# Optimization experiments

Hardware: AMD Instinct MI355X
Metric: run time of the kernel (lower is better)

The kernel has to match this reference:

```python
import jax, jax.numpy as jnp
import numpy as np

TOP_K = 2
EPS = 1e-9


def setup_inputs() -> dict:
    key = jax.random.key(0)
    ks = jax.random.split(key, 5)
    B, S, D, H, E, G = 4, 2048, 1024, 1024, 8, 256
    x = jax.random.normal(ks[0], (B, S, D), dtype=jnp.float32)
    # gate MLP (top_k_gating with hidden_size=gating_size)
    Wg1 = jax.random.normal(ks[1], (D, G), dtype=jnp.float32) * (1.0 / np.sqrt(D))
    Wg2 = jax.random.normal(ks[2], (G, E), dtype=jnp.float32) * (1.0 / np.sqrt(G))
    # experts: uniform(-1/D, 1/D) as in init_experts
    W_in = jax.random.uniform(ks[3], (E, D, H), dtype=jnp.float32, minval=-1.0 / D, maxval=1.0 / D)
    W_out = jax.random.uniform(ks[4], (E, H, D), dtype=jnp.float32, minval=-1.0 / D, maxval=1.0 / D)
    return {"x": x, "Wg1": Wg1, "Wg2": Wg2, "W_in": W_in, "W_out": W_out}


def _gate(xf, Wg1, Wg2):
    # gate MLP -> softmax probs over experts
    h = jnp.tanh(xf @ Wg1)                      # [N, G]
    probs = jax.nn.softmax(h @ Wg2, axis=-1)    # [N, E]
    top_v, top_i = jax.lax.top_k(probs, TOP_K)  # [N, k]
    N, E = probs.shape
    # dense gate matrix: zeros except top-k entries (== compute_gating combine weights)
    gates = jnp.zeros((N, E), probs.dtype).at[jnp.arange(N)[:, None], top_i].set(top_v)
    return gates, probs


def _mi_loss(probs):
    # mutual-information aux loss: minimize -(H(mean_p) - mean H(p))
    p_mean = probs.mean(axis=0)
    h_mean = -jnp.sum(p_mean * jnp.log(p_mean + EPS))
    mean_h = -jnp.mean(jnp.sum(probs * jnp.log(probs + EPS), axis=-1))
    return -h_mean + mean_h


def reference(x, Wg1, Wg2, W_in, W_out):
    B, S, D = x.shape
    xf = x.reshape(-1, D)                        # [N, D]
    gates, probs = _gate(xf, Wg1, Wg2)           # [N, E]
    # per-expert FFN: relu(x @ W_in[e]) @ W_out[e], combined with top-k gates.
    h = jnp.einsum('nd,edh->enh', xf, W_in)      # [E, N, H]
    h = jax.nn.relu(h)
    y = jnp.einsum('enh,ehd->end', h, W_out)     # [E, N, D]
    out = jnp.einsum('ne,end->nd', gates, y)     # gate-weighted combine
    loss = _mi_loss(probs)
    return out.reshape(B, S, D), loss
```

## Files before the change

kernel.cpp:

```cpp
#include <hip/hip_runtime.h>


#define N_TOK 8192
#define DIM   1024
#define HID   1024
#define NEXP  8
#define GDIM  256
#define NPAIR (N_TOK * 2)
#define HB_ROWS (NPAIR + 256)
#define MT2   72
#define GAP_P 5e-4f
#define SPLIT_SCALE 2048.0f

typedef __attribute__((ext_vector_type(4))) float    f32x4;
typedef __attribute__((ext_vector_type(8))) _Float16 f16x8;

static __device__ __forceinline__ void async_ld16(const void* g, void* l) {
  __builtin_amdgcn_global_load_lds(
      (const __attribute__((address_space(1))) unsigned int*)g,
      (__attribute__((address_space(3))) unsigned int*)l, 16, 0, 0);
}

__global__ void cast_x_kernel(const float* __restrict__ x, _Float16* __restrict__ xh,
                              _Float16* __restrict__ xl) {
  size_t o = ((size_t)blockIdx.x * 256 + threadIdx.x) * 8;
  float4 v0 = *(const float4*)(x + o);
  float4 v1 = *(const float4*)(x + o + 4);
  float v[8] = {v0.x, v0.y, v0.z, v0.w, v1.x, v1.y, v1.z, v1.w};
  f16x8 h, l;
#pragma unroll
  for (int k = 0; k < 8; ++k) {
    _Float16 hi = (_Float16)v[k];
    h[k] = hi;
    l[k] = (_Float16)((v[k] - (float)hi) * SPLIT_SCALE);
  }
  *(f16x8*)(xh + o) = h;
  *(f16x8*)(xl + o) = l;
}

__global__ __launch_bounds__(256) void cast_wg1_kernel(const float* __restrict__ Wg1,
                                                       _Float16* __restrict__ WhT,
                                                       _Float16* __restrict__ WlT) {
  __shared__ float t[64][65];
  int k0 = blockIdx.x * 64, g0 = blockIdx.y * 64;
  int tid = threadIdx.x;
  int col4 = tid & 15, ib = tid >> 4;
#pragma unroll
  for (int q = 0; q < 4; ++q) {
    int i = ib * 4 + q;
    *(float4*)&t[i][col4 * 4] = *(const float4*)&Wg1[(size_t)(k0 + i) * GDIM + g0 + col4 * 4];
  }
  __syncthreads();
#pragma unroll
  for (int q = 0; q < 2; ++q) {
    int c = tid * 2 + q;
    int j = c >> 3, i8 = (c & 7) * 8;
    f16x8 h, l;
#pragma unroll
    for (int k = 0; k < 8; ++k) {
      float v = t[i8 + k][j];
      _Float16 hi = (_Float16)v;
      h[k] = hi;
      l[k] = (_Float16)((v - (float)hi) * SPLIT_SCALE);
    }
    *(f16x8*)&WhT[(size_t)(g0 + j) * DIM + k0 + i8] = h;
    *(f16x8*)&WlT[(size_t)(g0 + j) * DIM + k0 + i8] = l;
  }
}

__global__ __launch_bounds__(256) void cast_wT_kernel(const float* __restrict__ Win,
                                                      const float* __restrict__ Wout,
                                                      _Float16* __restrict__ WinT,
                                                      _Float16* __restrict__ WoutT) {
  __shared__ float t[64][65];
  int z = blockIdx.z;
  const float* src = (z < NEXP ? Win : Wout) + (size_t)(z & 7) * DIM * HID;
  _Float16*    dst = (z < NEXP ? WinT : WoutT) + (size_t)(z & 7) * DIM * HID;
  int i0 = blockIdx.x * 64, j0 = blockIdx.y * 64;
  int tid = threadIdx.x;
  int col4 = tid & 15, ib = tid >> 4;
#pragma unroll
  for (int q = 0; q < 4; ++q) {
    int i = ib * 4 + q;
    *(float4*)&t[i][col4 * 4] = *(const float4*)&src[(size_t)(i0 + i) * 1024 + j0 + col4 * 4];
  }
  __syncthreads();
#pragma unroll
  for (int q = 0; q < 2; ++q) {
    int c = tid * 2 + q;
    int j = c >> 3, i8 = (c & 7) * 8;
    f16x8 h;
#pragma unroll
    for (int k = 0; k < 8; ++k) h[k] = (_Float16)t[i8 + k][j];
    *(f16x8*)&dst[(size_t)(j0 + j) * 1024 + i0 + i8] = h;
  }
}

__global__ __launch_bounds__(256) void gemm_hm_kernel(const _Float16* __restrict__ xh,
                                                      const _Float16* __restrict__ xl,
                                                      const _Float16* __restrict__ WhT,
                                                      const _Float16* __restrict__ WlT,
                                                      float* __restrict__ hg) {
  __shared__ __align__(16) _Float16 Ah[32 * 32], Al[32 * 32];
  __shared__ __align__(16) _Float16 Bh[128 * 32], Bl[128 * 32];
  int m0 = blockIdx.x * 32, n0 = blockIdx.y * 128;
  int tid = threadIdx.x, lane = tid & 63, wave = tid >> 6;
  int wr = (wave >> 1) * 16, wc = (wave & 1) * 64;
  int sel = tid >> 7, tt = tid & 127;
  int arow = tt >> 2;
  int aslot = (tt & 3) ^ ((tt >> 4) & 3);
  const _Float16* asrcp = (sel ? xl : xh) + (size_t)(m0 + arow) * DIM + aslot * 8;
  _Float16* adst = (sel ? Al : Ah) + (size_t)tt * 8;
  int brow = tid >> 2;
  int bslot = (tid & 3) ^ ((tid >> 4) & 3);
  size_t boff = (size_t)(n0 + brow) * DIM + bslot * 8;
  const size_t bo2 = (size_t)64 * DIM;
  int rdoff = ((lane >> 4) ^ ((lane >> 2) & 3)) << 3;
  f32x4 acc[4] = {}, accl[4] = {};
  for (int k0 = 0; k0 < DIM; k0 += 32) {
    __syncthreads();
    async_ld16(asrcp + k0, adst);
    async_ld16(WhT + boff + k0, Bh + (size_t)tid * 8);
    async_ld16(WhT + boff + bo2 + k0, Bh + (size_t)(256 + tid) * 8);
    async_ld16(WlT + boff + k0, Bl + (size_t)tid * 8);
    async_ld16(WlT + boff + bo2 + k0, Bl + (size_t)(256 + tid) * 8);
    __syncthreads();
    f16x8 a  = *(const f16x8*)&Ah[(wr + (lane & 15)) * 32 + rdoff];
    f16x8 al = *(const f16x8*)&Al[(wr + (lane & 15)) * 32 + rdoff];
#pragma unroll
    for (int n = 0; n < 4; ++n) {
      f16x8 b  = *(const f16x8*)&Bh[(wc + n * 16 + (lane & 15)) * 32 + rdoff];
      f16x8 bl = *(const f16x8*)&Bl[(wc + n * 16 + (lane & 15)) * 32 + rdoff];
      acc[n]  = __builtin_amdgcn_mfma_f32_16x16x32_f16(a, b, acc[n], 0, 0, 0);
      accl[n] = __builtin_amdgcn_mfma_f32_16x16x32_f16(al, b, accl[n], 0, 0, 0);
      accl[n] = __builtin_amdgcn_mfma_f32_16x16x32_f16(a, bl, accl[n], 0, 0, 0);
    }
  }
#pragma unroll
  for (int n = 0; n < 4; ++n) {
#pragma unroll
    for (int i = 0; i < 4; ++i) {
      int row = wr + ((lane >> 4) << 2) + i;
      int col = wc + n * 16 + (lane & 15);
      float v = acc[n][i] + accl[n][i] * (1.0f / SPLIT_SCALE);
      hg[(size_t)(m0 + row) * GDIM + n0 + col] = tanhf(v);
    }
  }
}

__global__ void gate_kernel(const float* __restrict__ hg, const float* __restrict__ Wg2,
                            int* __restrict__ top_i, float* __restrict__ top_v,
                            float* __restrict__ lossacc, int* __restrict__ counts,
                            int* __restrict__ nflag, int* __restrict__ flaglist) {
  __shared__ float psum[8];
  __shared__ float entsum;
  __shared__ int cnts[8];
  int tid = threadIdx.x;
  if (tid < 8) { psum[tid] = 0.f; cnts[tid] = 0; }
  if (tid == 0) entsum = 0.f;
  __syncthreads();
  int token = blockIdx.x * 8 + (tid >> 5);
  int lane = tid & 31;
  const float* hrow = hg + (size_t)token * GDIM;
  float lg[8] = {0, 0, 0, 0, 0, 0, 0, 0};
#pragma unroll
  for (int j = 0; j < 8; ++j) {
    int g = lane + (j << 5);
    float hv = hrow[g];
#pragma unroll
    for (int e = 0; e < 8; ++e) lg[e] = fmaf(hv, Wg2[g * 8 + e], lg[e]);
  }
#pragma unroll
  for (int e = 0; e < 8; ++e) {
    lg[e] += __shfl_xor(lg[e], 16);
    lg[e] += __shfl_xor(lg[e], 8);
    lg[e] += __shfl_xor(lg[e], 4);
    lg[e] += __shfl_xor(lg[e], 2);
    lg[e] += __shfl_xor(lg[e], 1);
  }
  if (lane == 0) {
    float mx = lg[0];
#pragma unroll
    for (int e = 1; e < 8; ++e) mx = fmaxf(mx, lg[e]);
    float p[8], s = 0.f;
#pragma unroll
    for (int e = 0; e < 8; ++e) { p[e] = expf(lg[e] - mx); s += p[e]; }
    float inv = 1.f / s, ent = 0.f;
    int i0 = 0, i1 = 0;
    float v0 = -1.f, v1 = -1.f, v2 = -1.f;
#pragma unroll
    for (int e = 0; e < 8; ++e) {
      p[e] *= inv;
      ent += p[e] * logf(p[e] + 1e-9f);
      if (p[e] > v0)      { v2 = v1; v1 = v0; i1 = i0; v0 = p[e]; i0 = e; }
      else if (p[e] > v1) { v2 = v1; v1 = p[e]; i1 = e; }
      else if (p[e] > v2) { v2 = p[e]; }
    }
    top_i[token * 2 + 0] = i0; top_i[token * 2 + 1] = i1;
    top_v[token * 2 + 0] = v0; top_v[token * 2 + 1] = v1;
    if (v1 - v2 < GAP_P) {
      int ix = atomicAdd(nflag, 1);
      if (ix < 8192) flaglist[ix] = token;
    }
#pragma unroll
    for (int e = 0; e < 8; ++e) atomicAdd(&psum[e], p[e]);
    atomicAdd(&entsum, ent);
    atomicAdd(&cnts[i0], 1);
    atomicAdd(&cnts[i1], 1);
  }
  __syncthreads();
  if (tid < 8) { atomicAdd(&lossacc[tid], psum[tid]); atomicAdd(&counts[tid], cnts[tid]); }
  if (tid == 8) atomicAdd(&lossacc[8], entsum);
}

__global__ __launch_bounds__(256) void regate_kernel(const float* __restrict__ x,
                                                     const float* __restrict__ Wg1,
                                                     const float* __restrict__ Wg2,
                                                     const int* __restrict__ nflag,
                                                     const int* __restrict__ flaglist,
                                                     int* __restrict__ top_i,
                                                     float* __restrict__ top_v,
                                                     int* __restrict__ counts) {
  __shared__ float xs[DIM];
  __shared__ float wsum[4][8];
  int tid = threadIdx.x;
  int nf = *nflag; if (nf > 8192) nf = 8192;
  for (int it = blockIdx.x; it < nf; it += gridDim.x) {
    int token = flaglist[it];
    const float* xr = x + (size_t)token * DIM;
    *(float4*)&xs[tid * 4] = *(const float4*)&xr[tid * 4];
    __syncthreads();
    float s0 = 0.f, s1 = 0.f, s2 = 0.f, s3 = 0.f;
    float s4 = 0.f, s5 = 0.f, s6 = 0.f, s7 = 0.f;
    for (int k = 0; k < DIM; k += 8) {
      s0 = fmaf(xs[k + 0], Wg1[(size_t)(k + 0) * GDIM + tid], s0);
      s1 = fmaf(xs[k + 1], Wg1[(size_t)(k + 1) * GDIM + tid], s1);
      s2 = fmaf(xs[k + 2], Wg1[(size_t)(k + 2) * GDIM + tid], s2);
      s3 = fmaf(xs[k + 3], Wg1[(size_t)(k + 3) * GDIM + tid], s3);
      s4 = fmaf(xs[k + 4], Wg1[(size_t)(k + 4) * GDIM + tid], s4);
      s5 = fmaf(xs[k + 5], Wg1[(size_t)(k + 5) * GDIM + tid], s5);
      s6 = fmaf(xs[k + 6], Wg1[(size_t)(k + 6) * GDIM + tid], s6);
      s7 = fmaf(xs[k + 7], Wg1[(size_t)(k + 7) * GDIM + tid], s7);
    }
    float hgv = tanhf(((s0 + s1) + (s2 + s3)) + ((s4 + s5) + (s6 + s7)));
    float lg[8];
#pragma unroll
    for (int e = 0; e < 8; ++e) lg[e] = hgv * Wg2[tid * 8 + e];
#pragma unroll
    for (int e = 0; e < 8; ++e) {
      lg[e] += __shfl_xor(lg[e], 32);
      lg[e] += __shfl_xor(lg[e], 16);
      lg[e] += __shfl_xor(lg[e], 8);
      lg[e] += __shfl_xor(lg[e], 4);
      lg[e] += __shfl_xor(lg[e], 2);
      lg[e] += __shfl_xor(lg[e], 1);
    }
    int wv = tid >> 6;
    if ((tid & 63) == 0) {
#pragma unroll
      for (int e = 0; e < 8; ++e) wsum[wv][e] = lg[e];
    }
    __syncthreads();
    if (tid == 0) {
      float l[8];
#pragma unroll
      for (int e = 0; e < 8; ++e)
        l[e] = (wsum[0][e] + wsum[1][e]) + (wsum[2][e] + wsum[3][e]);
      float mx = l[0];
#pragma unroll
      for (int e = 1; e < 8; ++e) mx = fmaxf(mx, l[e]);
      float p[8], s = 0.f;
#pragma unroll
      for (int e = 0; e < 8; ++e) { p[e] = expf(l[e] - mx); s += p[e]; }
      float inv = 1.f / s;
      int i0 = 0, i1 = 0;
      float v0 = -1.f, v1 = -1.f;
#pragma unroll
      for (int e = 0; e < 8; ++e) {
        p[e] *= inv;
        if (p[e] > v0)      { v1 = v0; i1 = i0; v0 = p[e]; i0 = e; }
        else if (p[e] > v1) { v1 = p[e]; i1 = e; }
      }
      int oi0 = top_i[token * 2 + 0], oi1 = top_i[token * 2 + 1];
      if (oi0 != i0 || oi1 != i1) {
        atomicSub(&counts[oi0], 1); atomicSub(&counts[oi1], 1);
        atomicAdd(&counts[i0], 1);  atomicAdd(&counts[i1], 1);
      }
      top_i[token * 2 + 0] = i0; top_i[token * 2 + 1] = i1;
      top_v[token * 2 + 0] = v0; top_v[token * 2 + 1] = v1;
    }
    __syncthreads();
  }
}

__global__ void scan_kernel(const int* __restrict__ counts, int* __restrict__ offsets) {
  if (threadIdx.x == 0) {
    int acc = 0;
#pragma unroll
    for (int e = 0; e < 8; ++e) { offsets[e] = acc; acc += counts[e]; }
    offsets[8] = acc;
  }
}

__global__ __launch_bounds__(256) void fill_kernel(const int* __restrict__ top_i,
                                                   const float* __restrict__ top_v,
                                                   const int* __restrict__ offsets,
                                                   int* __restrict__ cursors,
                                                   int* __restrict__ ptok,
                                                   float* __restrict__ pgate,
                                                   int* __restrict__ rowof) {
  __shared__ int lcnt[8];
  __shared__ int lbase[8];
  int tid = threadIdx.x;
  int n = blockIdx.x * 256 + tid;
  if (tid < 8) lcnt[tid] = 0;
  __syncthreads();
  int e0 = top_i[n * 2 + 0], e1 = top_i[n * 2 + 1];
  int p0 = atomicAdd(&lcnt[e0], 1);
  int p1 = atomicAdd(&lcnt[e1], 1);
  __syncthreads();
  if (tid < 8) lbase[tid] = atomicAdd(&cursors[tid], lcnt[tid]);
  __syncthreads();
  int r0 = offsets[e0] + lbase[e0] + p0;
  int r1 = offsets[e1] + lbase[e1] + p1;
  ptok[r0] = n;  pgate[r0] = top_v[n * 2 + 0];  rowof[n * 2 + 0] = r0;
  ptok[r1] = n;  pgate[r1] = top_v[n * 2 + 1];  rowof[n * 2 + 1] = r1;
}


__global__ __launch_bounds__(512) void gemm1_kernel(const _Float16* __restrict__ xh,
                                                    const _Float16* __restrict__ WinT,
                                                    _Float16* __restrict__ hb,
                                                    const int* __restrict__ offsets,
                                                    const int* __restrict__ ptok) {
  __shared__ __align__(16) _Float16 Als[2][256 * 32];
  __shared__ __align__(16) _Float16 Bls[2][128 * 32];
  int bx = blockIdx.x;
  int loc = (bx & 7) * 9 + (bx >> 3);
  int base = 0, cnt = 0, e;
  for (e = 0; e < NEXP; ++e) {
    base = offsets[e];
    cnt = offsets[e + 1] - base;
    int mts = (cnt + 255) >> 8;
    if (loc < mts) break;
    loc -= mts;
  }
  if (e == NEXP) return;
  int row0 = base + (loc << 8);
  int rmax = cnt - (loc << 8);
  int n0 = blockIdx.y << 7;
  int tid = threadIdx.x, wave = tid >> 6, lane = tid & 63;
  int wr = (wave >> 1) << 6;
  int wc = (wave & 1) << 6;

  const _Float16* WB = WinT + (size_t)e * DIM * HID;
  int scol = (((lane & 3) ^ (lane >> 4)) << 3);
  size_t asrc[2];
#pragma unroll
  for (int j = 0; j < 2; ++j) {
    int r = wave * 32 + j * 16 + (lane >> 2);
    int tok = ptok[(r < rmax) ? (row0 + r) : base];
    asrc[j] = (size_t)tok * DIM + scol;
  }
  int brow = tid >> 2;
  size_t bsrc = (size_t)(n0 + brow) * DIM + (((tid & 3) ^ ((tid >> 4) & 3)) << 3);
  int aldst = wave * 1024;
  int bldst = wave * 512;
  int rdoff = ((lane >> 4) ^ ((lane >> 2) & 3)) << 3;
  f32x4 acc[4][4] = {};

#pragma unroll
  for (int j = 0; j < 2; ++j) async_ld16(xh + asrc[j], &Als[0][aldst + j * 512]);
  async_ld16(WB + bsrc, &Bls[0][bldst]);
  __syncthreads();
  int c = 0;
  for (int k0 = 32; k0 <= DIM; k0 += 32) {
    if (k0 < DIM) {
#pragma unroll
      for (int j = 0; j < 2; ++j) async_ld16(xh + asrc[j] + k0, &Als[1 - c][aldst + j * 512]);
      async_ld16(WB + bsrc + k0, &Bls[1 - c][bldst]);
    }
    f16x8 a[4], b[4];
#pragma unroll
    for (int m = 0; m < 4; ++m)
      a[m] = *(const f16x8*)&Als[c][(wr + m * 16 + (lane & 15)) * 32 + rdoff];
#pragma unroll
    for (int n = 0; n < 4; ++n)
      b[n] = *(const f16x8*)&Bls[c][(wc + n * 16 + (lane & 15)) * 32 + rdoff];
#pragma unroll
    for (int m = 0; m < 4; ++m)
#pragma unroll
      for (int n = 0; n < 4; ++n)
        acc[m][n] = __builtin_amdgcn_mfma_f32_16x16x32_f16(a[m], b[n], acc[m][n], 0, 0, 0);
    __syncthreads();
    c ^= 1;
  }
#pragma unroll
  for (int m = 0; m < 4; ++m) {
#pragma unroll
    for (int i = 0; i < 4; ++i) {
      int r = wr + m * 16 + ((lane >> 4) << 2) + i;
      if (r < rmax) {
        _Float16* hrow = hb + (size_t)(row0 + r) * HID;
#pragma unroll
        for (int n = 0; n < 4; ++n)
          hrow[n0 + wc + n * 16 + (lane & 15)] = (_Float16)fmaxf(acc[m][n][i], 0.f);
      }
    }
  }
}

__global__ __launch_bounds__(512) void gemm2_kernel(const _Float16* __restrict__ hb,
                                                    const _Float16* __restrict__ WoutT,
                                                    _Float16* __restrict__ yb,
                                                    const int* __restrict__ offsets,
                                                    const float* __restrict__ pgate) {
  __shared__ __align__(16) _Float16 Als[2][256 * 32];
  __shared__ __align__(16) _Float16 Bls[2][128 * 32];
  int bx = blockIdx.x;
  int loc = (bx & 7) * 9 + (bx >> 3);
  int base = 0, cnt = 0, e;
  for (e = 0; e < NEXP; ++e) {
    base = offsets[e];
    cnt = offsets[e + 1] - base;
    int mts = (cnt + 255) >> 8;
    if (loc < mts) break;
    loc -= mts;
  }
  if (e == NEXP) return;
  int row0 = base + (loc << 8);
  int rmax = cnt - (loc << 8);
  int n0 = blockIdx.y << 7;
  int tid = threadIdx.x, wave = tid >> 6, lane = tid & 63;
  int wr = (wave >> 1) << 6, wc = (wave & 1) << 6;

  const _Float16* WB = WoutT + (size_t)e * DIM * HID;
  int scol = (((lane & 3) ^ (lane >> 4)) << 3);
  size_t asrc[2];
#pragma unroll
  for (int j = 0; j < 2; ++j) {
    int r = wave * 32 + j * 16 + (lane >> 2);
    asrc[j] = (size_t)(row0 + r) * HID + scol;
  }
  int brow = tid >> 2;
  size_t bsrc = (size_t)(n0 + brow) * DIM + (((tid & 3) ^ ((tid >> 4) & 3)) << 3);
  int aldst = wave * 1024;
  int bldst = wave * 512;
  int rdoff = ((lane >> 4) ^ ((lane >> 2) & 3)) << 3;
  f32x4 acc[4][4] = {};

#pragma unroll
  for (int j = 0; j < 2; ++j) async_ld16(hb + asrc[j], &Als[0][aldst + j * 512]);
  async_ld16(WB + bsrc, &Bls[0][bldst]);
  __syncthreads();
  int c = 0;
  for (int k0 = 32; k0 <= HID; k0 += 32) {
    if (k0 < HID) {
#pragma unroll
      for (int j = 0; j < 2; ++j) async_ld16(hb + asrc[j] + k0, &Als[1 - c][aldst + j * 512]);
      async_ld16(WB + bsrc + k0, &Bls[1 - c][bldst]);
    }
    f16x8 a[4], b[4];
#pragma unroll
    for (int m = 0; m < 4; ++m)
      a[m] = *(const f16x8*)&Als[c][(wr + m * 16 + (lane & 15)) * 32 + rdoff];
#pragma unroll
    for (int n = 0; n < 4; ++n)
      b[n] = *(const f16x8*)&Bls[c][(wc + n * 16 + (lane & 15)) * 32 + rdoff];
#pragma unroll
    for (int m = 0; m < 4; ++m)
#pragma unroll
      for (int n = 0; n < 4; ++n)
        acc[m][n] = __builtin_amdgcn_mfma_f32_16x16x32_f16(a[m], b[n], acc[m][n], 0, 0, 0);
    __syncthreads();
    c ^= 1;
  }
#pragma unroll
  for (int m = 0; m < 4; ++m) {
#pragma unroll
    for (int i = 0; i < 4; ++i) {
      int r = wr + m * 16 + ((lane >> 4) << 2) + i;
      if (r < rmax) {
        int gr = row0 + r;
        float gv = pgate[gr];
        _Float16* yrow = yb + (size_t)gr * DIM;
#pragma unroll
        for (int n = 0; n < 4; ++n)
          yrow[n0 + wc + n * 16 + (lane & 15)] = (_Float16)(gv * acc[m][n][i]);
      }
    }
  }
}

__global__ __launch_bounds__(256) void combine_kernel(const _Float16* __restrict__ yb,
                                                      const int* __restrict__ rowof,
                                                      float* __restrict__ out) {
  int tid = threadIdx.x;
  int token = blockIdx.x * 2 + (tid >> 7);
  int d0 = (tid & 127) * 8;
  int r0 = rowof[token * 2 + 0];
  int r1 = rowof[token * 2 + 1];
  f16x8 a = *(const f16x8*)&yb[(size_t)r0 * DIM + d0];
  f16x8 b = *(const f16x8*)&yb[(size_t)r1 * DIM + d0];
  float* orow = out + (size_t)token * DIM + d0;
  float4 o0, o1;
  o0.x = (float)a[0] + (float)b[0]; o0.y = (float)a[1] + (float)b[1];
  o0.z = (float)a[2] + (float)b[2]; o0.w = (float)a[3] + (float)b[3];
  o1.x = (float)a[4] + (float)b[4]; o1.y = (float)a[5] + (float)b[5];
  o1.z = (float)a[6] + (float)b[6]; o1.w = (float)a[7] + (float)b[7];
  *(float4*)orow = o0;
  *(float4*)(orow + 4) = o1;
}

__global__ void loss_kernel(const float* __restrict__ lossacc, float* __restrict__ dst) {
  if (threadIdx.x == 0 && blockIdx.x == 0) {
    float t1 = 0.f;
#pragma unroll
    for (int e = 0; e < 8; ++e) {
      float pm = lossacc[e] * (1.f / (float)N_TOK);
      t1 += pm * logf(pm + 1e-9f);
    }
    dst[0] = t1 - lossacc[8] * (1.f / (float)N_TOK);
  }
}

extern "C" void kernel_launch(void* const* d_in, const int* in_sizes, int n_in,
                              void* d_out, int out_size, void* d_ws, size_t ws_size,
                              hipStream_t stream) {
  const float* x    = (const float*)d_in[0];
  const float* Wg1  = (const float*)d_in[1];
  const float* Wg2  = (const float*)d_in[2];
  const float* Win  = (const float*)d_in[3];
  const float* Wout = (const float*)d_in[4];
  float* out = (float*)d_out;

  char* ws = (char*)d_ws;
  size_t off = 0;
  auto alloc = [&](size_t bytes) -> void* {
    void* p = ws + off;
    off = (off + bytes + 255) & ~(size_t)255;
    return p;
  };
  int*   counts  = (int*)alloc(32);
  int*   offsets = (int*)alloc(64);
  int*   cursors = (int*)alloc(32);
  float* lossacc = (float*)alloc(64);
  int*   nflag   = (int*)alloc(32);
  int*   flaglist= (int*)alloc(8192 * 4);
  int*   top_i   = (int*)alloc((size_t)NPAIR * 4);
  float* top_v   = (float*)alloc((size_t)NPAIR * 4);
  int*   ptok    = (int*)alloc((size_t)NPAIR * 4);
  float* pgate   = (float*)alloc((size_t)NPAIR * 4);
  int*   rowof   = (int*)alloc((size_t)NPAIR * 4);
  float* hg      = (float*)alloc((size_t)N_TOK * GDIM * 4);
  char*  scratch1 = (char*)alloc((size_t)HB_ROWS * HID * 2);
  _Float16* xl     = (_Float16*)scratch1;
  _Float16* Wg1hT  = (_Float16*)(scratch1 + (size_t)N_TOK * DIM * 2);
  _Float16* Wg1lsT = Wg1hT + (size_t)GDIM * DIM;
  _Float16* hb     = (_Float16*)scratch1;
  _Float16* xh    = (_Float16*)alloc((size_t)N_TOK * DIM * 2);
  _Float16* WinT  = (_Float16*)alloc((size_t)NEXP * DIM * HID * 2);
  _Float16* WoutT = (_Float16*)alloc((size_t)NEXP * DIM * HID * 2);
  _Float16* yb = xh;
  (void)ws_size; (void)in_sizes; (void)n_in;

  hipMemsetAsync(d_ws, 0, 2048, stream);

  cast_x_kernel<<<N_TOK * DIM / (8 * 256), 256, 0, stream>>>(x, xh, xl);
  cast_wg1_kernel<<<dim3(DIM / 64, GDIM / 64), 256, 0, stream>>>(Wg1, Wg1hT, Wg1lsT);
  cast_wT_kernel<<<dim3(16, 16, 16), 256, 0, stream>>>(Win, Wout, WinT, WoutT);
  gemm_hm_kernel<<<dim3(N_TOK / 32, GDIM / 128), 256, 0, stream>>>(xh, xl, Wg1hT, Wg1lsT, hg);
  gate_kernel<<<N_TOK / 8, 256, 0, stream>>>(hg, Wg2, top_i, top_v, lossacc, counts,
                                             nflag, flaglist);
  regate_kernel<<<256, 256, 0, stream>>>(x, Wg1, Wg2, nflag, flaglist, top_i, top_v, counts);
  scan_kernel<<<1, 32, 0, stream>>>(counts, offsets);
  fill_kernel<<<N_TOK / 256, 256, 0, stream>>>(top_i, top_v, offsets, cursors, ptok, pgate, rowof);
  gemm1_kernel<<<dim3(MT2, HID / 128), 512, 0, stream>>>(xh, WinT, hb, offsets, ptok);
  gemm2_kernel<<<dim3(MT2, DIM / 128), 512, 0, stream>>>(hb, WoutT, yb, offsets, pgate);
  combine_kernel<<<N_TOK / 2, 256, 0, stream>>>(yb, rowof, out);
  loss_kernel<<<1, 64, 0, stream>>>(lossacc, out + (size_t)N_TOK * DIM);
}
```

Before: 267.9 us.

## Merge prep casts, drop scan/loss launches, restructure expert GEMM double-buffer pipeline

Merges three cast kernels into one prep kernel and folds the offset scan into fill and the GEMM tile lookup. The loss finalisation moves into the combine kernel, removing several small launches. The expert GEMMs get a rewritten double-buffered pipeline that prefetches two stages ahead. It uses explicit vmcnt waits, barriers and MFMA priority raising so loads overlap compute. The pipeline depends on hand-tuned waitcnt counts and risks races if they are off.

```diff
diff --git a/kernel.cpp b/kernel.cpp
--- a/kernel.cpp
+++ b/kernel.cpp
@@ -21,78 +21,80 @@
       (__attribute__((address_space(3))) unsigned int*)l, 16, 0, 0);
 }
 
-__global__ void cast_x_kernel(const float* __restrict__ x, _Float16* __restrict__ xh,
-                              _Float16* __restrict__ xl) {
-  size_t o = ((size_t)blockIdx.x * 256 + threadIdx.x) * 8;
-  float4 v0 = *(const float4*)(x + o);
-  float4 v1 = *(const float4*)(x + o + 4);
-  float v[8] = {v0.x, v0.y, v0.z, v0.w, v1.x, v1.y, v1.z, v1.w};
-  f16x8 h, l;
-#pragma unroll
-  for (int k = 0; k < 8; ++k) {
-    _Float16 hi = (_Float16)v[k];
-    h[k] = hi;
-    l[k] = (_Float16)((v[k] - (float)hi) * SPLIT_SCALE);
-  }
-  *(f16x8*)(xh + o) = h;
-  *(f16x8*)(xl + o) = l;
-}
-
-__global__ __launch_bounds__(256) void cast_wg1_kernel(const float* __restrict__ Wg1,
-                                                       _Float16* __restrict__ WhT,
-                                                       _Float16* __restrict__ WlT) {
+__global__ __launch_bounds__(256) void prep_kernel(const float* __restrict__ x,
+                                                   _Float16* __restrict__ xh,
+                                                   _Float16* __restrict__ xl,
+                                                   const float* __restrict__ Wg1,
+                                                   _Float16* __restrict__ WhT,
+                                                   _Float16* __restrict__ WlT,
+                                                   const float* __restrict__ Win,
+                                                   const float* __restrict__ Wout,
+                                                   _Float16* __restrict__ WinT,
+                                                   _Float16* __restrict__ WoutT) {
   __shared__ float t[64][65];
-  int k0 = blockIdx.x * 64, g0 = blockIdx.y * 64;
+  int bx = blockIdx.x;
   int tid = threadIdx.x;
-  int col4 = tid & 15, ib = tid >> 4;
-#pragma unroll
-  for (int q = 0; q < 4; ++q) {
-    int i = ib * 4 + q;
-    *(float4*)&t[i][col4 * 4] = *(const float4*)&Wg1[(size_t)(k0 + i) * GDIM + g0 + col4 * 4];
-  }
-  __syncthreads();
-#pragma unroll
-  for (int q = 0; q < 2; ++q) {
-    int c = tid * 2 + q;
-    int j = c >> 3, i8 = (c & 7) * 8;
+  if (bx < 4096) {
+    size_t o = ((size_t)bx * 256 + tid) * 8;
+    float4 v0 = *(const float4*)(x + o);
+    float4 v1 = *(const float4*)(x + o + 4);
+    float v[8] = {v0.x, v0.y, v0.z, v0.w, v1.x, v1.y, v1.z, v1.w};
     f16x8 h, l;
 #pragma unroll
     for (int k = 0; k < 8; ++k) {
-      float v = t[i8 + k][j];
-      _Float16 hi = (_Float16)v;
+      _Float16 hi = (_Float16)v[k];
       h[k] = hi;
-      l[k] = (_Float16)((v - (float)hi) * SPLIT_SCALE);
-    }
-    *(f16x8*)&WhT[(size_t)(g0 + j) * DIM + k0 + i8] = h;
-    *(f16x8*)&WlT[(size_t)(g0 + j) * DIM + k0 + i8] = l;
-  }
-}
-
-__global__ __launch_bounds__(256) void cast_wT_kernel(const float* __restrict__ Win,
-                                                      const float* __restrict__ Wout,
-                                                      _Float16* __restrict__ WinT,
-                                                      _Float16* __restrict__ WoutT) {
-  __shared__ float t[64][65];
-  int z = blockIdx.z;
-  const float* src = (z < NEXP ? Win : Wout) + (size_t)(z & 7) * DIM * HID;
-  _Float16*    dst = (z < NEXP ? WinT : WoutT) + (size_t)(z & 7) * DIM * HID;
-  int i0 = blockIdx.x * 64, j0 = blockIdx.y * 64;
-  int tid = threadIdx.x;
-  int col4 = tid & 15, ib = tid >> 4;
-#pragma unroll
-  for (int q = 0; q < 4; ++q) {
-    int i = ib * 4 + q;
-    *(float4*)&t[i][col4 * 4] = *(const float4*)&src[(size_t)(i0 + i) * 1024 + j0 + col4 * 4];
-  }
-  __syncthreads();
-#pragma unroll
-  for (int q = 0; q < 2; ++q) {
-    int c = tid * 2 + q;
-    int j = c >> 3, i8 = (c & 7) * 8;
-    f16x8 h;
-#pragma unroll
-    for (int k = 0; k < 8; ++k) h[k] = (_Float16)t[i8 + k][j];
-    *(f16x8*)&dst[(size_t)(j0 + j) * 1024 + i0 + i8] = h;
+      l[k] = (_Float16)((v[k] - (float)hi) * SPLIT_SCALE);
+    }
+    *(f16x8*)(xh + o) = h;
+    *(f16x8*)(xl + o) = l;
+  } else if (bx < 4096 + 64) {
+    int b = bx - 4096;
+    int k0 = (b & 15) * 64, g0 = (b >> 4) * 64;
+    int col4 = tid & 15, ib = tid >> 4;
+#pragma unroll
+    for (int q = 0; q < 4; ++q) {
+      int i = ib * 4 + q;
+      *(float4*)&t[i][col4 * 4] = *(const float4*)&Wg1[(size_t)(k0 + i) * GDIM + g0 + col4 * 4];
+    }
+    __syncthreads();
+#pragma unroll
+    for (int q = 0; q < 2; ++q) {
+      int c = tid * 2 + q;
+      int j = c >> 3, i8 = (c & 7) * 8;
+      f16x8 h, l;
+#pragma unroll
+      for (int k = 0; k < 8; ++k) {
+        float v = t[i8 + k][j];
+        _Float16 hi = (_Float16)v;
+        h[k] = hi;
+        l[k] = (_Float16)((v - (float)hi) * SPLIT_SCALE);
+      }
+      *(f16x8*)&WhT[(size_t)(g0 + j) * DIM + k0 + i8] = h;
+      *(f16x8*)&WlT[(size_t)(g0 + j) * DIM + k0 + i8] = l;
+    }
+  } else {
+    int b = bx - 4160;
+    int z = b >> 8, rem = b & 255;
+    const float* src = (z < NEXP ? Win : Wout) + (size_t)(z & 7) * DIM * HID;
+    _Float16*    dst = (z < NEXP ? WinT : WoutT) + (size_t)(z & 7) * DIM * HID;
+    int i0 = (rem & 15) * 64, j0 = (rem >> 4) * 64;
+    int col4 = tid & 15, ib = tid >> 4;
+#pragma unroll
+    for (int q = 0; q < 4; ++q) {
+      int i = ib * 4 + q;
+      *(float4*)&t[i][col4 * 4] = *(const float4*)&src[(size_t)(i0 + i) * 1024 + j0 + col4 * 4];
+    }
+    __syncthreads();
+#pragma unroll
+    for (int q = 0; q < 2; ++q) {
+      int c = tid * 2 + q;
+      int j = c >> 3, i8 = (c & 7) * 8;
+      f16x8 h;
+#pragma unroll
+      for (int k = 0; k < 8; ++k) h[k] = (_Float16)t[i8 + k][j];
+      *(f16x8*)&dst[(size_t)(j0 + j) * 1024 + i0 + i8] = h;
+    }
   }
 }
 
@@ -293,26 +295,23 @@
   }
 }
 
-__global__ void scan_kernel(const int* __restrict__ counts, int* __restrict__ offsets) {
-  if (threadIdx.x == 0) {
-    int acc = 0;
-#pragma unroll
-    for (int e = 0; e < 8; ++e) { offsets[e] = acc; acc += counts[e]; }
-    offsets[8] = acc;
-  }
-}
-
 __global__ __launch_bounds__(256) void fill_kernel(const int* __restrict__ top_i,
                                                    const float* __restrict__ top_v,
-                                                   const int* __restrict__ offsets,
+                                                   const int* __restrict__ counts,
                                                    int* __restrict__ cursors,
                                                    int* __restrict__ ptok,
                                                    float* __restrict__ pgate,
                                                    int* __restrict__ rowof) {
   __shared__ int lcnt[8];
   __shared__ int lbase[8];
+  __shared__ int soff[8];
   int tid = threadIdx.x;
   int n = blockIdx.x * 256 + tid;
+  if (tid == 0) {
+    int a = 0;
+#pragma unroll
+    for (int e = 0; e < 8; ++e) { soff[e] = a; a += counts[e]; }
+  }
   if (tid < 8) lcnt[tid] = 0;
   __syncthreads();
   int e0 = top_i[n * 2 + 0], e1 = top_i[n * 2 + 1];
@@ -321,17 +320,50 @@
   __syncthreads();
   if (tid < 8) lbase[tid] = atomicAdd(&cursors[tid], lcnt[tid]);
   __syncthreads();
-  int r0 = offsets[e0] + lbase[e0] + p0;
-  int r1 = offsets[e1] + lbase[e1] + p1;
+  int r0 = soff[e0] + lbase[e0] + p0;
+  int r1 = soff[e1] + lbase[e1] + p1;
   ptok[r0] = n;  pgate[r0] = top_v[n * 2 + 0];  rowof[n * 2 + 0] = r0;
   ptok[r1] = n;  pgate[r1] = top_v[n * 2 + 1];  rowof[n * 2 + 1] = r1;
 }
 
+
+#define GEMM_PIPE(STAGE_EXPR)                                                        \
+  STAGE_EXPR(0, 0);                                                                  \
+  STAGE_EXPR(32, 1);                                                                 \
+  asm volatile("s_waitcnt vmcnt(3)" ::: "memory");                                   \
+  __builtin_amdgcn_s_barrier();                                                      \
+  int cbuf = 0;                                                                      \
+  for (int t = 0; t < 32; ++t) {                                                     \
+    f16x8 a[4], b[4];                                                                \
+    _Pragma("unroll")                                                                \
+    for (int m = 0; m < 4; ++m)                                                      \
+      a[m] = *(const f16x8*)&Als[cbuf][(wr + m * 16 + (lane & 15)) * 32 + rdoff];    \
+    _Pragma("unroll")                                                                \
+    for (int n = 0; n < 4; ++n)                                                      \
+      b[n] = *(const f16x8*)&Bls[cbuf][(wc + n * 16 + (lane & 15)) * 32 + rdoff];    \
+    asm volatile("s_waitcnt lgkmcnt(0)" ::: "memory");                               \
+    __builtin_amdgcn_sched_barrier(0);                                               \
+    __builtin_amdgcn_s_barrier();                                                    \
+    bool st = (t + 2 < 32);                                                          \
+    if (st) { STAGE_EXPR((t + 2) * 32, cbuf); }                                      \
+    __builtin_amdgcn_s_setprio(1);                                                   \
+    _Pragma("unroll")                                                                \
+    for (int m = 0; m < 4; ++m)                                                      \
+      _Pragma("unroll")                                                              \
+      for (int n = 0; n < 4; ++n)                                                    \
+        acc[m][n] = __builtin_amdgcn_mfma_f32_16x16x32_f16(a[m], b[n], acc[m][n], 0, 0, 0); \
+    __builtin_amdgcn_s_setprio(0);                                                   \
+    if (st) asm volatile("s_waitcnt vmcnt(3)" ::: "memory");                         \
+    else    asm volatile("s_waitcnt vmcnt(0)" ::: "memory");                         \
+    __builtin_amdgcn_sched_barrier(0);                                               \
+    __builtin_amdgcn_s_barrier();                                                    \
+    cbuf ^= 1;                                                                       \
+  }
 
 __global__ __launch_bounds__(512) void gemm1_kernel(const _Float16* __restrict__ xh,
                                                     const _Float16* __restrict__ WinT,
                                                     _Float16* __restrict__ hb,
-                                                    const int* __restrict__ offsets,
+                                                    const int* __restrict__ counts,
                                                     const int* __restrict__ ptok) {
   __shared__ __align__(16) _Float16 Als[2][256 * 32];
   __shared__ __align__(16) _Float16 Bls[2][128 * 32];
@@ -339,19 +371,17 @@
   int loc = (bx & 7) * 9 + (bx >> 3);
   int base = 0, cnt = 0, e;
   for (e = 0; e < NEXP; ++e) {
-    base = offsets[e];
-    cnt = offsets[e + 1] - base;
+    cnt = counts[e];
     int mts = (cnt + 255) >> 8;
     if (loc < mts) break;
-    loc -= mts;
+    loc -= mts; base += cnt;
   }
   if (e == NEXP) return;
   int row0 = base + (loc << 8);
   int rmax = cnt - (loc << 8);
   int n0 = blockIdx.y << 7;
   int tid = threadIdx.x, wave = tid >> 6, lane = tid & 63;
-  int wr = (wave >> 1) << 6;
-  int wc = (wave & 1) << 6;
+  int wr = (wave >> 1) << 6, wc = (wave & 1) << 6;
 
   const _Float16* WB = WinT + (size_t)e * DIM * HID;
   int scol = (((lane & 3) ^ (lane >> 4)) << 3);
@@ -369,32 +399,16 @@
   int rdoff = ((lane >> 4) ^ ((lane >> 2) & 3)) << 3;
   f32x4 acc[4][4] = {};
 
-#pragma unroll
-  for (int j = 0; j < 2; ++j) async_ld16(xh + asrc[j], &Als[0][aldst + j * 512]);
-  async_ld16(WB + bsrc, &Bls[0][bldst]);
-  __syncthreads();
-  int c = 0;
-  for (int k0 = 32; k0 <= DIM; k0 += 32) {
-    if (k0 < DIM) {
-#pragma unroll
-      for (int j = 0; j < 2; ++j) async_ld16(xh + asrc[j] + k0, &Als[1 - c][aldst + j * 512]);
-      async_ld16(WB + bsrc + k0, &Bls[1 - c][bldst]);
-    }
-    f16x8 a[4], b[4];
-#pragma unroll
-    for (int m = 0; m < 4; ++m)
-      a[m] = *(const f16x8*)&Als[c][(wr + m * 16 + (lane & 15)) * 32 + rdoff];
-#pragma unroll
-    for (int n = 0; n < 4; ++n)
-      b[n] = *(const f16x8*)&Bls[c][(wc + n * 16 + (lane & 15)) * 32 + rdoff];
-#pragma unroll
-    for (int m = 0; m < 4; ++m)
-#pragma unroll
-      for (int n = 0; n < 4; ++n)
-        acc[m][n] = __builtin_amdgcn_mfma_f32_16x16x32_f16(a[m], b[n], acc[m][n], 0, 0, 0);
-    __syncthreads();
-    c ^= 1;
-  }
+#define STAGE1(K0, CB)                                          \
+  do {                                                          \
+    async_ld16(xh + asrc[0] + (K0), &Als[(CB)][aldst]);         \
+    async_ld16(xh + asrc[1] + (K0), &Als[(CB)][aldst + 512]);   \
+    async_ld16(WB + bsrc + (K0), &Bls[(CB)][bldst]);            \
+  } while (0)
+
+  GEMM_PIPE(STAGE1)
+#undef STAGE1
+
 #pragma unroll
   for (int m = 0; m < 4; ++m) {
 #pragma unroll
@@ -413,7 +427,7 @@
 __global__ __launch_bounds__(512) void gemm2_kernel(const _Float16* __restrict__ hb,
                                                     const _Float16* __restrict__ WoutT,
                                                     _Float16* __restrict__ yb,
-                                                    const int* __restrict__ offsets,
+                                                    const int* __restrict__ counts,
                                                     const float* __restrict__ pgate) {
   __shared__ __align__(16) _Float16 Als[2][256 * 32];
   __shared__ __align__(16) _Float16 Bls[2][128 * 32];
@@ -421,11 +435,10 @@
   int loc = (bx & 7) * 9 + (bx >> 3);
   int base = 0, cnt = 0, e;
   for (e = 0; e < NEXP; ++e) {
-    base = offsets[e];
-    cnt = offsets[e + 1] - base;
+    cnt = counts[e];
     int mts = (cnt + 255) >> 8;
     if (loc < mts) break;
-    loc -= mts;
+    loc -= mts; base += cnt;
   }
   if (e == NEXP) return;
   int row0 = base + (loc << 8);
@@ -449,32 +462,16 @@
   int rdoff = ((lane >> 4) ^ ((lane >> 2) & 3)) << 3;
   f32x4 acc[4][4] = {};
 
-#pragma unroll
-  for (int j = 0; j < 2; ++j) async_ld16(hb + asrc[j], &Als[0][aldst + j * 512]);
-  async_ld16(WB + bsrc, &Bls[0][bldst]);
-  __syncthreads();
-  int c = 0;
-  for (int k0 = 32; k0 <= HID; k0 += 32) {
-    if (k0 < HID) {
-#pragma unroll
-      for (int j = 0; j < 2; ++j) async_ld16(hb + asrc[j] + k0, &Als[1 - c][aldst + j * 512]);
-      async_ld16(WB + bsrc + k0, &Bls[1 - c][bldst]);
-    }
-    f16x8 a[4], b[4];
-#pragma unroll
-    for (int m = 0; m < 4; ++m)
-      a[m] = *(const f16x8*)&Als[c][(wr + m * 16 + (lane & 15)) * 32 + rdoff];
-#pragma unroll
-    for (int n = 0; n < 4; ++n)
-      b[n] = *(const f16x8*)&Bls[c][(wc + n * 16 + (lane & 15)) * 32 + rdoff];
-#pragma unroll
-    for (int m = 0; m < 4; ++m)
-#pragma unroll
-      for (int n = 0; n < 4; ++n)
-        acc[m][n] = __builtin_amdgcn_mfma_f32_16x16x32_f16(a[m], b[n], acc[m][n], 0, 0, 0);
-    __syncthreads();
-    c ^= 1;
-  }
+#define STAGE2(K0, CB)                                          \
+  do {                                                          \
+    async_ld16(hb + asrc[0] + (K0), &Als[(CB)][aldst]);         \
+    async_ld16(hb + asrc[1] + (K0), &Als[(CB)][aldst + 512]);   \
+    async_ld16(WB + bsrc + (K0), &Bls[(CB)][bldst]);            \
+  } while (0)
+
+  GEMM_PIPE(STAGE2)
+#undef STAGE2
+
 #pragma unroll
   for (int m = 0; m < 4; ++m) {
 #pragma unroll
@@ -494,7 +491,9 @@
 
 __global__ __launch_bounds__(256) void combine_kernel(const _Float16* __restrict__ yb,
                                                       const int* __restrict__ rowof,
-                                                      float* __restrict__ out) {
+                                                      float* __restrict__ out,
+                                                      const float* __restrict__ lossacc,
+                                                      float* __restrict__ lossdst) {
   int tid = threadIdx.x;
   int token = blockIdx.x * 2 + (tid >> 7);
   int d0 = (tid & 127) * 8;
@@ -510,17 +509,14 @@
   o1.z = (float)a[6] + (float)b[6]; o1.w = (float)a[7] + (float)b[7];
   *(float4*)orow = o0;
   *(float4*)(orow + 4) = o1;
-}
-
-__global__ void loss_kernel(const float* __restrict__ lossacc, float* __restrict__ dst) {
-  if (threadIdx.x == 0 && blockIdx.x == 0) {
+  if (blockIdx.x == 0 && tid == 0) {
     float t1 = 0.f;
 #pragma unroll
     for (int e = 0; e < 8; ++e) {
       float pm = lossacc[e] * (1.f / (float)N_TOK);
       t1 += pm * logf(pm + 1e-9f);
     }
-    dst[0] = t1 - lossacc[8] * (1.f / (float)N_TOK);
+    lossdst[0] = t1 - lossacc[8] * (1.f / (float)N_TOK);
   }
 }
 
@@ -542,7 +538,6 @@
     return p;
   };
   int*   counts  = (int*)alloc(32);
-  int*   offsets = (int*)alloc(64);
   int*   cursors = (int*)alloc(32);
   float* lossacc = (float*)alloc(64);
   int*   nflag   = (int*)alloc(32);
@@ -566,17 +561,16 @@
 
   hipMemsetAsync(d_ws, 0, 2048, stream);
 
-  cast_x_kernel<<<N_TOK * DIM / (8 * 256), 256, 0, stream>>>(x, xh, xl);
-  cast_wg1_kernel<<<dim3(DIM / 64, GDIM / 64), 256, 0, stream>>>(Wg1, Wg1hT, Wg1lsT);
-  cast_wT_kernel<<<dim3(16, 16, 16), 256, 0, stream>>>(Win, Wout, WinT, WoutT);
+  prep_kernel<<<4096 + 64 + 4096, 256, 0, stream>>>(x, xh, xl, Wg1, Wg1hT, Wg1lsT,
+                                                    Win, Wout, WinT, WoutT);
   gemm_hm_kernel<<<dim3(N_TOK / 32, GDIM / 128), 256, 0, stream>>>(xh, xl, Wg1hT, Wg1lsT, hg);
   gate_kernel<<<N_TOK / 8, 256, 0, stream>>>(hg, Wg2, top_i, top_v, lossacc, counts,
                                              nflag, flaglist);
   regate_kernel<<<256, 256, 0, stream>>>(x, Wg1, Wg2, nflag, flaglist, top_i, top_v, counts);
-  scan_kernel<<<1, 32, 0, stream>>>(counts, offsets);
-  fill_kernel<<<N_TOK / 256, 256, 0, stream>>>(top_i, top_v, offsets, cursors, ptok, pgate, rowof);
-  gemm1_kernel<<<dim3(MT2, HID / 128), 512, 0, stream>>>(xh, WinT, hb, offsets, ptok);
-  gemm2_kernel<<<dim3(MT2, DIM / 128), 512, 0, stream>>>(hb, WoutT, yb, offsets, pgate);
-  combine_kernel<<<N_TOK / 2, 256, 0, stream>>>(yb, rowof, out);
-  loss_kernel<<<1, 64, 0, stream>>>(lossacc, out + (size_t)N_TOK * DIM);
-}
+  fill_kernel<<<N_TOK / 256, 256, 0, stream>>>(top_i, top_v, counts, cursors,
+                                               ptok, pgate, rowof);
+  gemm1_kernel<<<dim3(MT2, HID / 128), 512, 0, stream>>>(xh, WinT, hb, counts, ptok);
+  gemm2_kernel<<<dim3(MT2, DIM / 128), 512, 0, stream>>>(hb, WoutT, yb, counts, pgate);
+  combine_kernel<<<N_TOK / 2, 256, 0, stream>>>(yb, rowof, out, lossacc,
+                                                out + (size_t)N_TOK * DIM);
+}
```

Measured after the change: 261.5 us. 2.4% less time.
